# Kernel tuning notes

Hardware: AMD Instinct MI355X
Metric: run time of the kernel (lower is better)

Reference implementation:

```python
import jax, jax.numpy as jnp
import numpy as np


def setup_inputs() -> dict:
    key = jax.random.key(0)
    k1, k2 = jax.random.split(key)
    x = jax.random.normal(k1, (16, 128, 64, 64), dtype=jnp.float32)
    # weight layout: [out_channels, in_channels, kh, kw], kernel must be 3 for the
    # original Python-loop bounds to match the allocated output size
    weight = jax.random.normal(k2, (256, 128, 3, 3), dtype=jnp.float32) * 0.05
    return {"x": x, "weight": weight}


def reference(x, weight):
    # Stride-1 conv2d with symmetric zero padding=1 (forward ignores bias/stride/
    # dilation/groups in the original module).
    pad = 1
    out = jax.lax.conv_general_dilated(
        x, weight,
        window_strides=(1, 1),
        padding=[(pad, pad), (pad, pad)],
        dimension_numbers=("NCHW", "OIHW", "NCHW"),
    )
    return out
```

## Files before the change

### kernel.cpp

```cpp
#include <hip/hip_runtime.h>
#include <hip/hip_bf16.h>
#include <stdint.h>

typedef short bf16x8 __attribute__((ext_vector_type(8)));
typedef float f32x16 __attribute__((ext_vector_type(16)));

#define N_IMG 16
#define C_IN  128
#define H_IMG 64
#define W_IMG 64
#define K_OUT 256

#define XB_BYTES (16ull*66*66*128*2)
#define WB_BYTES (36ull*8*2*64*16)
#define WS_NEED  (XB_BYTES + WB_BYTES)

#define LDSX_BYTES (4*66*256)

__device__ __forceinline__ void gload16(void* lds, const void* g) {
    __builtin_amdgcn_global_load_lds(
        (const __attribute__((address_space(1))) void*)g,
        (__attribute__((address_space(3))) void*)lds, 16, 0, 0);
}

__device__ __forceinline__ uint32_t pack2(float a, float b) {
    __hip_bfloat16 ha = __float2bfloat16(a), hb = __float2bfloat16(b);
    return (uint32_t)*(uint16_t*)&ha | ((uint32_t)*(uint16_t*)&hb << 16);
}

__global__ __launch_bounds__(256)
void transform_fused_kernel(const float* __restrict__ x, const float* __restrict__ w,
                            __hip_bfloat16* __restrict__ xb, __hip_bfloat16* __restrict__ wb) {
    __shared__ __align__(16) uint32_t xs[64 * 64];
    __shared__ float lw[1152];
    const int b = blockIdx.x;
    const int t = threadIdx.x;

    if (b < 1056) {
        const int yt = b % 66;
        const int n  = b / 66;
        const bool interior = (yt >= 1 && yt <= 64);

        if (interior) {
            const float4* src = (const float4*)(x + (size_t)n * 524288 + (size_t)(yt - 1) * 64);
            #pragma unroll
            for (int it = 0; it < 4; ++it) {
                const int x4 = t & 15;
                const int j  = (t >> 4) + it * 16;
                float4 va = src[(2 * j) * 1024 + x4];
                float4 vb = src[(2 * j + 1) * 1024 + x4];
                const float* pa = (const float*)&va;
                const float* pb = (const float*)&vb;
                #pragma unroll
                for (int i = 0; i < 4; ++i) {
                    int row = x4 * 4 + i;
                    xs[row * 64 + (j ^ (((row >> 2) & 3) << 2))] = pack2(pa[i], pb[i]);
                }
            }
        }
        __syncthreads();

        uint4* dst = (uint4*)((char*)xb + (size_t)(n * 66 + yt) * 66 * 256);
        #pragma unroll
        for (int it = 0; it < 5; ++it) {
            int ch = t + it * 256;
            if (ch < 1056) {
                int xt = ch >> 4, u = ch & 15;
                uint4 val = make_uint4(0u, 0u, 0u, 0u);
                if (interior && xt >= 1 && xt <= 64) {
                    int row = xt - 1;
                    val = *(const uint4*)&xs[row * 64 + 4 * (u ^ ((row >> 2) & 3))];
                }
                dst[ch] = val;
            }
        }
    } else {
        const int kg = b - 1056;
        for (int e = t; e < 1152; e += 256) lw[e] = w[kg * 1152 + e];
        __syncthreads();
        const int basek = (kg >> 5) * 1024 + (kg & 31) * 8;
        #pragma unroll
        for (int tap = 0; tap < 9; ++tap) {
            if (t < 128) {
                int c = t;
                int idx = (tap * 4 + (c >> 5)) * 8192 + basek
                        + ((c >> 4) & 1) * 512 + ((c >> 3) & 1) * 256 + (c & 7);
                wb[idx] = __float2bfloat16(lw[c * 9 + tap]);
            }
        }
    }
}

#define DO_CHUNK(J, AUSE, ALOAD, RS66)                                                        \
  {                                                                                           \
    int jn = (J) + 1; if (jn >= 36) jn = 0;                                                   \
    const char* wc = wgw + (size_t)jn * 16384;                                                \
    _Pragma("unroll") for (int kf = 0; kf < 2; ++kf)                                          \
      _Pragma("unroll") for (int ks = 0; ks < 2; ++ks)                                        \
        ALOAD[kf][ks] = *(const bf16x8*)(wc + kf * 2048 + ks * 1024);                         \
    const int cc_ = (J) & 3;                                                                  \
    _Pragma("unroll") for (int ks = 0; ks < 2; ++ks) {                                        \
      bf16x8 xv[2];                                                                           \
      _Pragma("unroll") for (int f = 0; f < 2; ++f) {                                         \
        int rc  = rc0[f] + (RS66);                                                            \
        int off = cc_ * 64 + ks * 32 + hi4;                                                   \
        xv[f] = *(const bf16x8*)(lds + rc * 256 + (off ^ ((rc & 7) << 4)));                   \
      }                                                                                       \
      __builtin_amdgcn_s_setprio(1);                                                          \
      _Pragma("unroll") for (int kf = 0; kf < 2; ++kf)                                        \
        _Pragma("unroll") for (int f = 0; f < 2; ++f)                                         \
          acc[kf][f] = __builtin_amdgcn_mfma_f32_32x32x16_bf16(AUSE[kf][ks], xv[f],           \
                                                               acc[kf][f], 0, 0, 0);         \
      __builtin_amdgcn_s_setprio(0);                                                          \
    }                                                                                         \
  }

__global__ __launch_bounds__(512, 4)
void conv3x3_mfma_kernel(const char* __restrict__ xg,
                         const char* __restrict__ wg2,
                         float* __restrict__ out) {
    __shared__ uint4 smem[LDSX_BYTES / 16];
    char* lds = (char*)smem;

    const int t    = threadIdx.x;
    const int b    = blockIdx.x;
    const int yp   = b & 31;
    const int n    = b >> 5;
    const int lane = t & 63;
    const int wv   = t >> 6;
    const int lm   = lane & 31;
    const int hi   = lane >> 5;
    const int kb   = (wv & 3) * 64;
    const int mb   = (wv >> 2) * 64;
    const int hi4  = hi * 16;

    int rc0[2];
    #pragma unroll
    for (int f = 0; f < 2; ++f) {
        int m = mb + f * 32 + lm;
        rc0[f] = (m >> 6) * 66 + (m & 63);
    }

    const char* xsrc = xg + (size_t)(n * 66 + yp * 2) * 66 * 256;
    for (int ch = t; ch < LDSX_BYTES / 16; ch += 512) {
        int L = ch * 16;
        gload16(lds + L, xsrc + (L ^ (((L >> 8) & 7) << 4)));
    }

    const char* wgw = wg2 + (kb >> 5) * 2048 + lane * 16;
    bf16x8 aA[2][2], aB[2][2];
    #pragma unroll
    for (int kf = 0; kf < 2; ++kf)
        #pragma unroll
        for (int ks = 0; ks < 2; ++ks)
            aA[kf][ks] = *(const bf16x8*)(wgw + kf * 2048 + ks * 1024);

    asm volatile("s_waitcnt vmcnt(0)" ::: "memory");
    __syncthreads();

    f32x16 acc[2][2];
    #pragma unroll
    for (int i = 0; i < 2; ++i)
        #pragma unroll
        for (int j = 0; j < 2; ++j)
            acc[i][j] = (f32x16)(0.f);

    for (int tap = 0; tap < 9; ++tap) {
        const int r    = (tap >= 6) ? 2 : (tap >= 3 ? 1 : 0);
        const int rs66 = r * 66 + (tap - r * 3);
        const int j0   = tap * 4;
        DO_CHUNK(j0 + 0, aA, aB, rs66)
        DO_CHUNK(j0 + 1, aB, aA, rs66)
        DO_CHUNK(j0 + 2, aA, aB, rs66)
        DO_CHUNK(j0 + 3, aB, aA, rs66)
    }

    const int y0 = yp * 2;
    #pragma unroll
    for (int kf = 0; kf < 2; ++kf) {
        const int kbase2 = kb + kf * 32 + 4 * hi;
        #pragma unroll
        for (int f = 0; f < 2; ++f) {
            int m  = mb + f * 32 + lm;
            int yy = m >> 6;
            int xx = m & 63;
            float* op = out + (((size_t)(n * 256 + kbase2) * 64) + y0 + yy) * 64 + xx;
            #pragma unroll
            for (int reg = 0; reg < 16; ++reg) {
                int koff = (reg & 3) + 8 * (reg >> 2);
                op[(size_t)koff * 4096] = acc[kf][f][reg];
            }
        }
    }
}

__global__ __launch_bounds__(256, 3)
void conv3x3_f32_kernel(const float* __restrict__ x,
                        const float* __restrict__ w,
                        float* __restrict__ out) {
    __shared__ float xs[16][3][72];
    __shared__ float ws[16][9][64];

    const int t  = threadIdx.x;
    const int kt = blockIdx.x & 3;
    const int y  = (blockIdx.x >> 2) & 63;
    const int n  = blockIdx.x >> 8;

    const int k2   = t >> 3;
    const int xg   = t & 7;
    const int kloc = k2 * 2;
    const int x0   = xg * 8;

    float acc0[8] = {0.f,0.f,0.f,0.f,0.f,0.f,0.f,0.f};
    float acc1[8] = {0.f,0.f,0.f,0.f,0.f,0.f,0.f,0.f};

    const int k0 = kt * 64;

    for (int c0 = 0; c0 < C_IN; c0 += 16) {
        for (int idx = t; idx < 16 * 3 * 66; idx += 256) {
            int col = idx % 66;
            int rc  = idx / 66;
            int r   = rc % 3;
            int c   = rc / 3;
            int gx  = col - 1;
            int gy  = y - 1 + r;
            float v = 0.f;
            if ((unsigned)gx < (unsigned)W_IMG && (unsigned)gy < (unsigned)H_IMG)
                v = x[(((n * C_IN) + c0 + c) * H_IMG + gy) * W_IMG + gx];
            xs[c][r][col] = v;
        }
        for (int idx = t; idx < 64 * 16 * 9; idx += 256) {
            int tap = idx % 9;
            int ck  = idx / 9;
            int c   = ck % 16;
            int k   = ck / 16;
            ws[c][tap][k] = w[((k0 + k) * C_IN + c0 + c) * 9 + tap];
        }
        __syncthreads();

        #pragma unroll 2
        for (int c = 0; c < 16; ++c) {
            #pragma unroll
            for (int r = 0; r < 3; ++r) {
                float xr[10];
                #pragma unroll
                for (int i = 0; i < 10; ++i) xr[i] = xs[c][r][x0 + i];
                #pragma unroll
                for (int s = 0; s < 3; ++s) {
                    float w0 = ws[c][r * 3 + s][kloc];
                    float w1 = ws[c][r * 3 + s][kloc + 1];
                    #pragma unroll
                    for (int i = 0; i < 8; ++i) {
                        acc0[i] = fmaf(w0, xr[i + s], acc0[i]);
                        acc1[i] = fmaf(w1, xr[i + s], acc1[i]);
                    }
                }
            }
        }
        __syncthreads();
    }

    float* o0 = &out[(((n * K_OUT) + k0 + kloc) * H_IMG + y) * W_IMG + x0];
    float* o1 = o0 + H_IMG * W_IMG;
    #pragma unroll
    for (int i = 0; i < 8; ++i) o0[i] = acc0[i];
    #pragma unroll
    for (int i = 0; i < 8; ++i) o1[i] = acc1[i];
}

extern "C" void kernel_launch(void* const* d_in, const int* in_sizes, int n_in,
                              void* d_out, int out_size, void* d_ws, size_t ws_size,
                              hipStream_t stream) {
    const float* x = (const float*)d_in[0];
    const float* w = (const float*)d_in[1];
    float* out = (float*)d_out;
    (void)in_sizes; (void)n_in; (void)out_size;

    if (ws_size >= WS_NEED) {
        __hip_bfloat16* xb = (__hip_bfloat16*)d_ws;
        __hip_bfloat16* wb = (__hip_bfloat16*)((char*)d_ws + XB_BYTES);
        transform_fused_kernel<<<1056 + 256, 256, 0, stream>>>(x, w, xb, wb);
        conv3x3_mfma_kernel<<<512, 512, 0, stream>>>((const char*)xb, (const char*)wb, out);
    } else {
        conv3x3_f32_kernel<<<4096, 256, 0, stream>>>(x, w, out);
    }
}
```

Before: 132.8 us.

## Swizzle block order, widen LDS XOR swizzle, stagger per-wave weight chunk start

Block IDs are remapped so consecutive blocks land on different XCDs while blocks of the same image share L2. The LDS XOR swizzle widens from 8 to 16 rows to cut bank conflicts on the activation reads. Each wave now starts the 36-chunk reduction loop at a different chunk, spreading concurrent weight loads across addresses. The loop is rewritten as a rotating 18-iteration double buffer. This changes fp32 accumulation order per wave and adds some index arithmetic.

New measurement: 130.9 us. Within noise of the previous version (-1.4%).

```diff
diff --git a/kernel.cpp b/kernel.cpp
--- a/kernel.cpp
+++ b/kernel.cpp
@@ -91,28 +91,33 @@
     }
 }
 
-#define DO_CHUNK(J, AUSE, ALOAD, RS66)                                                        \
-  {                                                                                           \
-    int jn = (J) + 1; if (jn >= 36) jn = 0;                                                   \
-    const char* wc = wgw + (size_t)jn * 16384;                                                \
-    _Pragma("unroll") for (int kf = 0; kf < 2; ++kf)                                          \
-      _Pragma("unroll") for (int ks = 0; ks < 2; ++ks)                                        \
-        ALOAD[kf][ks] = *(const bf16x8*)(wc + kf * 2048 + ks * 1024);                         \
-    const int cc_ = (J) & 3;                                                                  \
-    _Pragma("unroll") for (int ks = 0; ks < 2; ++ks) {                                        \
-      bf16x8 xv[2];                                                                           \
-      _Pragma("unroll") for (int f = 0; f < 2; ++f) {                                         \
-        int rc  = rc0[f] + (RS66);                                                            \
-        int off = cc_ * 64 + ks * 32 + hi4;                                                   \
-        xv[f] = *(const bf16x8*)(lds + rc * 256 + (off ^ ((rc & 7) << 4)));                   \
-      }                                                                                       \
-      __builtin_amdgcn_s_setprio(1);                                                          \
-      _Pragma("unroll") for (int kf = 0; kf < 2; ++kf)                                        \
-        _Pragma("unroll") for (int f = 0; f < 2; ++f)                                         \
-          acc[kf][f] = __builtin_amdgcn_mfma_f32_32x32x16_bf16(AUSE[kf][ks], xv[f],           \
-                                                               acc[kf][f], 0, 0, 0);         \
-      __builtin_amdgcn_s_setprio(0);                                                          \
-    }                                                                                         \
+#define LOADW(DST, JJ)                                                    \
+  { const char* wc = wgw + (size_t)(JJ) * 16384;                          \
+    _Pragma("unroll") for (int kf = 0; kf < 2; ++kf)                      \
+      _Pragma("unroll") for (int ks = 0; ks < 2; ++ks)                    \
+        DST[kf][ks] = *(const bf16x8*)(wc + kf * 2048 + ks * 1024); }
+
+#define COMPUTE(JJ, AU)                                                   \
+  {                                                                       \
+    const int tap_ = (JJ) >> 2, cc_ = (JJ) & 3;                           \
+    const int r_   = (tap_ >= 6) ? 2 : ((tap_ >= 3) ? 1 : 0);             \
+    const int rs66 = tap_ + r_ * 63;                        \
+    const int scc  = hi4 ^ (cc_ << 6);                                    \
+    bf16x8 xv0[2], xv1[2];                                                \
+    _Pragma("unroll") for (int f = 0; f < 2; ++f) {                       \
+      int rc = rc0[f] + rs66;                                             \
+      int Lb = rc * 256 + (scc ^ ((rc & 15) << 4));                       \
+      xv0[f] = *(const bf16x8*)(lds + Lb);                                \
+      xv1[f] = *(const bf16x8*)(lds + (Lb ^ 32));                         \
+    }                                                                     \
+    __builtin_amdgcn_s_setprio(1);                                        \
+    _Pragma("unroll") for (int kf = 0; kf < 2; ++kf)                      \
+      _Pragma("unroll") for (int f = 0; f < 2; ++f)                       \
+        acc[kf][f] = __builtin_amdgcn_mfma_f32_32x32x16_bf16(AU[kf][0], xv0[f], acc[kf][f], 0, 0, 0); \
+    _Pragma("unroll") for (int kf = 0; kf < 2; ++kf)                      \
+      _Pragma("unroll") for (int f = 0; f < 2; ++f)                       \
+        acc[kf][f] = __builtin_amdgcn_mfma_f32_32x32x16_bf16(AU[kf][1], xv1[f], acc[kf][f], 0, 0, 0); \
+    __builtin_amdgcn_s_setprio(0);                                        \
   }
 
 __global__ __launch_bounds__(512, 4)
@@ -123,7 +128,8 @@
     char* lds = (char*)smem;
 
     const int t    = threadIdx.x;
-    const int b    = blockIdx.x;
+    const int b0   = blockIdx.x;
+    const int b    = ((b0 & 7) << 6) | (b0 >> 3);
     const int yp   = b & 31;
     const int n    = b >> 5;
     const int lane = t & 63;
@@ -144,16 +150,13 @@
     const char* xsrc = xg + (size_t)(n * 66 + yp * 2) * 66 * 256;
     for (int ch = t; ch < LDSX_BYTES / 16; ch += 512) {
         int L = ch * 16;
-        gload16(lds + L, xsrc + (L ^ (((L >> 8) & 7) << 4)));
-    }
-
-    const char* wgw = wg2 + (kb >> 5) * 2048 + lane * 16;
+        gload16(lds + L, xsrc + (L ^ (((L >> 8) & 15) << 4)));
+    }
+
+    const char* wgw = wg2 + (wv & 3) * 4096 + lane * 16;
+    const int start = wv * 4 + (wv >> 1);
     bf16x8 aA[2][2], aB[2][2];
-    #pragma unroll
-    for (int kf = 0; kf < 2; ++kf)
-        #pragma unroll
-        for (int ks = 0; ks < 2; ++ks)
-            aA[kf][ks] = *(const bf16x8*)(wgw + kf * 2048 + ks * 1024);
+    LOADW(aA, start)
 
     asm volatile("s_waitcnt vmcnt(0)" ::: "memory");
     __syncthreads();
@@ -165,14 +168,15 @@
         for (int j = 0; j < 2; ++j)
             acc[i][j] = (f32x16)(0.f);
 
-    for (int tap = 0; tap < 9; ++tap) {
-        const int r    = (tap >= 6) ? 2 : (tap >= 3 ? 1 : 0);
-        const int rs66 = r * 66 + (tap - r * 3);
-        const int j0   = tap * 4;
-        DO_CHUNK(j0 + 0, aA, aB, rs66)
-        DO_CHUNK(j0 + 1, aB, aA, rs66)
-        DO_CHUNK(j0 + 2, aA, aB, rs66)
-        DO_CHUNK(j0 + 3, aB, aA, rs66)
+    int j  = start;
+    int jn = (j + 1 == 36) ? 0 : j + 1;
+    for (int it = 0; it < 18; ++it) {
+        LOADW(aB, jn)
+        COMPUTE(j, aA)
+        j = jn; jn = (j + 1 == 36) ? 0 : j + 1;
+        LOADW(aA, jn)
+        COMPUTE(j, aB)
+        j = jn; jn = (j + 1 == 36) ? 0 : j + 1;
     }
 
     const int y0 = yp * 2;
```

## Use 4-wave blocks with wider per-wave M tile and triple-buffered weight prefetch

Applied to the files above, without the earlier changes.

Each block now runs 4 waves instead of 8, and each wave computes 64 output channels by 128 pixels instead of 64 by 64. Each weight fragment loaded from global memory is therefore reused across twice as many MFMAs, which halves per-block weight traffic. Weight registers are triple-buffered with a prefetch distance of two chunks, and the tap loop is fully unrolled with precomputed LDS addresses. The LDS XOR swizzle widens from 8 to 16 rows, and block indices are remapped to change cache locality. The cost is higher register pressure from 8 accumulators per wave and a launch bound of 2 blocks per CU, which lowers occupancy and latency hiding.

New measurement: 127.7 us. 3.8% less time.

```diff
diff --git a/kernel.cpp b/kernel.cpp
--- a/kernel.cpp
+++ b/kernel.cpp
@@ -91,31 +91,13 @@
     }
 }
 
-#define DO_CHUNK(J, AUSE, ALOAD, RS66)                                                        \
-  {                                                                                           \
-    int jn = (J) + 1; if (jn >= 36) jn = 0;                                                   \
-    const char* wc = wgw + (size_t)jn * 16384;                                                \
-    _Pragma("unroll") for (int kf = 0; kf < 2; ++kf)                                          \
-      _Pragma("unroll") for (int ks = 0; ks < 2; ++ks)                                        \
-        ALOAD[kf][ks] = *(const bf16x8*)(wc + kf * 2048 + ks * 1024);                         \
-    const int cc_ = (J) & 3;                                                                  \
-    _Pragma("unroll") for (int ks = 0; ks < 2; ++ks) {                                        \
-      bf16x8 xv[2];                                                                           \
-      _Pragma("unroll") for (int f = 0; f < 2; ++f) {                                         \
-        int rc  = rc0[f] + (RS66);                                                            \
-        int off = cc_ * 64 + ks * 32 + hi4;                                                   \
-        xv[f] = *(const bf16x8*)(lds + rc * 256 + (off ^ ((rc & 7) << 4)));                   \
-      }                                                                                       \
-      __builtin_amdgcn_s_setprio(1);                                                          \
-      _Pragma("unroll") for (int kf = 0; kf < 2; ++kf)                                        \
-        _Pragma("unroll") for (int f = 0; f < 2; ++f)                                         \
-          acc[kf][f] = __builtin_amdgcn_mfma_f32_32x32x16_bf16(AUSE[kf][ks], xv[f],           \
-                                                               acc[kf][f], 0, 0, 0);         \
-      __builtin_amdgcn_s_setprio(0);                                                          \
-    }                                                                                         \
-  }
-
-__global__ __launch_bounds__(512, 4)
+#define LOADW(DST, JJ)                                                     \
+  { const char* wc_ = wgw + (size_t)(JJ) * 16384;                          \
+    _Pragma("unroll") for (int kf_ = 0; kf_ < 2; ++kf_)                    \
+      _Pragma("unroll") for (int ks_ = 0; ks_ < 2; ++ks_)                  \
+        DST[kf_][ks_] = *(const bf16x8*)(wc_ + kf_ * 2048 + ks_ * 1024); }
+
+__global__ __launch_bounds__(256, 2)
 void conv3x3_mfma_kernel(const char* __restrict__ xg,
                          const char* __restrict__ wg2,
                          float* __restrict__ out) {
@@ -123,56 +105,85 @@
     char* lds = (char*)smem;
 
     const int t    = threadIdx.x;
-    const int b    = blockIdx.x;
+    const int b0   = blockIdx.x;
+    const int b    = ((b0 & 7) << 6) | (b0 >> 3);
     const int yp   = b & 31;
     const int n    = b >> 5;
     const int lane = t & 63;
     const int wv   = t >> 6;
     const int lm   = lane & 31;
     const int hi   = lane >> 5;
-    const int kb   = (wv & 3) * 64;
-    const int mb   = (wv >> 2) * 64;
+    const int kb   = wv * 64;
     const int hi4  = hi * 16;
 
-    int rc0[2];
-    #pragma unroll
-    for (int f = 0; f < 2; ++f) {
-        int m = mb + f * 32 + lm;
+    int rc0[4];
+    #pragma unroll
+    for (int f = 0; f < 4; ++f) {
+        int m = f * 32 + lm;
         rc0[f] = (m >> 6) * 66 + (m & 63);
     }
 
     const char* xsrc = xg + (size_t)(n * 66 + yp * 2) * 66 * 256;
-    for (int ch = t; ch < LDSX_BYTES / 16; ch += 512) {
+    for (int ch = t; ch < LDSX_BYTES / 16; ch += 256) {
         int L = ch * 16;
-        gload16(lds + L, xsrc + (L ^ (((L >> 8) & 7) << 4)));
-    }
-
-    const char* wgw = wg2 + (kb >> 5) * 2048 + lane * 16;
-    bf16x8 aA[2][2], aB[2][2];
-    #pragma unroll
-    for (int kf = 0; kf < 2; ++kf)
-        #pragma unroll
-        for (int ks = 0; ks < 2; ++ks)
-            aA[kf][ks] = *(const bf16x8*)(wgw + kf * 2048 + ks * 1024);
+        gload16(lds + L, xsrc + (L ^ (((L >> 8) & 15) << 4)));
+    }
+
+    const char* wgw = wg2 + wv * 4096 + lane * 16;
+    bf16x8 aA[2][2], aB[2][2], aC[2][2];
+    LOADW(aA, 0)
+    LOADW(aB, 1)
 
     asm volatile("s_waitcnt vmcnt(0)" ::: "memory");
     __syncthreads();
 
-    f32x16 acc[2][2];
+    f32x16 acc[2][4];
     #pragma unroll
     for (int i = 0; i < 2; ++i)
         #pragma unroll
-        for (int j = 0; j < 2; ++j)
-            acc[i][j] = (f32x16)(0.f);
-
+        for (int jj = 0; jj < 4; ++jj)
+            acc[i][jj] = (f32x16)(0.f);
+
+    #pragma unroll
     for (int tap = 0; tap < 9; ++tap) {
-        const int r    = (tap >= 6) ? 2 : (tap >= 3 ? 1 : 0);
+        const int r    = (tap >= 6) ? 2 : ((tap >= 3) ? 1 : 0);
         const int rs66 = r * 66 + (tap - r * 3);
-        const int j0   = tap * 4;
-        DO_CHUNK(j0 + 0, aA, aB, rs66)
-        DO_CHUNK(j0 + 1, aB, aA, rs66)
-        DO_CHUNK(j0 + 2, aA, aB, rs66)
-        DO_CHUNK(j0 + 3, aB, aA, rs66)
+        int base[4];
+        #pragma unroll
+        for (int f = 0; f < 4; ++f) {
+            int rc = rc0[f] + rs66;
+            base[f] = rc * 256 + (hi4 ^ ((rc & 15) << 4));
+        }
+        #pragma unroll
+        for (int cc = 0; cc < 4; ++cc) {
+            const int j   = tap * 4 + cc;
+            const int jp2 = (j + 2 >= 36) ? (j + 2 - 36) : (j + 2);
+            bf16x8 (*AU)[2] = (j % 3 == 0) ? aA : ((j % 3 == 1) ? aB : aC);
+            bf16x8 (*AL)[2] = ((j + 2) % 3 == 0) ? aA : (((j + 2) % 3 == 1) ? aB : aC);
+            {
+                const char* wc_ = wgw + (size_t)jp2 * 16384;
+                #pragma unroll
+                for (int kf = 0; kf < 2; ++kf)
+                    #pragma unroll
+                    for (int ks = 0; ks < 2; ++ks)
+                        AL[kf][ks] = *(const bf16x8*)(wc_ + kf * 2048 + ks * 1024);
+            }
+            #pragma unroll
+            for (int ks = 0; ks < 2; ++ks) {
+                bf16x8 xv[4];
+                #pragma unroll
+                for (int f = 0; f < 4; ++f)
+                    xv[f] = *(const bf16x8*)(lds + (base[f] ^ (cc << 6) ^ (ks << 5)));
+                __builtin_amdgcn_s_setprio(1);
+                #pragma unroll
+                for (int kf = 0; kf < 2; ++kf)
+                    #pragma unroll
+                    for (int f = 0; f < 4; ++f)
+                        acc[kf][f] = __builtin_amdgcn_mfma_f32_32x32x16_bf16(
+                            AU[kf][ks], xv[f], acc[kf][f], 0, 0, 0);
+                __builtin_amdgcn_s_setprio(0);
+            }
+        }
     }
 
     const int y0 = yp * 2;
@@ -180,8 +191,8 @@
     for (int kf = 0; kf < 2; ++kf) {
         const int kbase2 = kb + kf * 32 + 4 * hi;
         #pragma unroll
-        for (int f = 0; f < 2; ++f) {
-            int m  = mb + f * 32 + lm;
+        for (int f = 0; f < 4; ++f) {
+            int m  = f * 32 + lm;
             int yy = m >> 6;
             int xx = m & 63;
             float* op = out + (((size_t)(n * 256 + kbase2) * 64) + y0 + yy) * 64 + xx;
@@ -280,7 +291,7 @@
         __hip_bfloat16* xb = (__hip_bfloat16*)d_ws;
         __hip_bfloat16* wb = (__hip_bfloat16*)((char*)d_ws + XB_BYTES);
         transform_fused_kernel<<<1056 + 256, 256, 0, stream>>>(x, w, xb, wb);
-        conv3x3_mfma_kernel<<<512, 512, 0, stream>>>((const char*)xb, (const char*)wb, out);
+        conv3x3_mfma_kernel<<<512, 256, 0, stream>>>((const char*)xb, (const char*)wb, out);
     } else {
         conv3x3_f32_kernel<<<4096, 256, 0, stream>>>(x, w, out);
     }
```
